# Kernel optimization log

Hardware: AMD Instinct MI355X
Metric: run time of the kernel (lower is better)

Reference implementation:

```python
import jax, jax.numpy as jnp
import numpy as np
from jax import lax

BN_EPS = 1e-5


def _conv(x, w):
    # stride-1, VALID conv; the torch 'locally connected' layer shares weights
    # across pixels, so it is exactly a standard conv2d.
    return lax.conv_general_dilated(
        x, w, window_strides=(1, 1), padding='VALID',
        dimension_numbers=('NCHW', 'OIHW', 'NCHW'))


def _batchnorm(x, gamma, beta):
    # training-mode BatchNorm2d: batch statistics over (N, H, W)
    mean = jnp.mean(x, axis=(0, 2, 3), keepdims=True)
    var = jnp.var(x, axis=(0, 2, 3), keepdims=True)
    xhat = (x - mean) * lax.rsqrt(var + BN_EPS)
    return xhat * gamma[None, :, None, None] + beta[None, :, None, None]


def setup_inputs() -> dict:
    key = jax.random.key(0)
    ks = jax.random.split(key, 6)
    B = 16384
    x = jax.random.normal(ks[0], (B, 256), dtype=jnp.float32)
    w1 = jax.random.normal(ks[1], (16, 1, 3, 3), dtype=jnp.float32)
    w2 = jax.random.normal(ks[2], (32, 16, 2, 2), dtype=jnp.float32)
    w3 = jax.random.normal(ks[3], (64, 32, 1, 1), dtype=jnp.float32)
    fan_in = 64 * 13 * 13
    bound = 1.0 / np.sqrt(fan_in)
    fc_w = jax.random.uniform(ks[4], (10, fan_in), minval=-bound, maxval=bound, dtype=jnp.float32)
    fc_b = jax.random.uniform(ks[5], (10,), minval=-bound, maxval=bound, dtype=jnp.float32)
    return {
        'x': x, 'w1': w1, 'w2': w2, 'w3': w3,
        'g1': jnp.ones((16,), jnp.float32), 'b1': jnp.zeros((16,), jnp.float32),
        'g2': jnp.ones((32,), jnp.float32), 'b2': jnp.zeros((32,), jnp.float32),
        'g3': jnp.ones((64,), jnp.float32), 'b3': jnp.zeros((64,), jnp.float32),
        'fc_w': fc_w, 'fc_b': fc_b,
    }


def reference(x, w1, w2, w3, g1, b1, g2, b2, g3, b3, fc_w, fc_b):
    h = x.reshape(-1, 1, 16, 16)                     # [B,1,16,16]
    h = jax.nn.relu(_batchnorm(_conv(h, w1), g1, b1))  # [B,16,14,14]
    h = jax.nn.relu(_batchnorm(_conv(h, w2), g2, b2))  # [B,32,13,13]
    h = jax.nn.relu(_batchnorm(_conv(h, w3), g3, b3))  # [B,64,13,13]
    h = h.reshape(h.shape[0], -1)                    # [B, 64*13*13]
    # dropout is identity in eval/deterministic mode
    return h @ fc_w.T + fc_b                         # [B,10]
```

## Files before the change

kernel.cpp:

```cpp
#include <hip/hip_runtime.h>


#define NPART 1024
#define P2_OFF 32768
#define ST_OFF 229376
#define ST1 ST_OFF
#define ST2 (ST_OFF + 32)
#define ST3 (ST_OFF + 96)
#define C2R_OFF 230400
#define C1R_OFF 231424
#define C2P_OFF 262144
#define A2G_BYTE 5242880ull
#define FCB_N 86528
#define A1S 24
#define A1B 384

typedef __attribute__((ext_vector_type(8))) short bf16x8;
typedef __attribute__((ext_vector_type(4))) float f32x4;
typedef __attribute__((ext_vector_type(4))) unsigned int u32x4;

__device__ __forceinline__ unsigned int f2bf(float f) {
  unsigned int u = __float_as_uint(f);
  return (u + 0x7fffu + ((u >> 16) & 1u)) >> 16;
}
__device__ __forceinline__ unsigned int pkbf(float a, float b) {
  unsigned ua = __float_as_uint(a) + 0x8000u;
  unsigned ub = __float_as_uint(b) + 0x8000u;
  return __builtin_amdgcn_perm(ub, ua, 0x07060302u);
}
__device__ __forceinline__ bf16x8 mkfrag(uint2 a, uint2 b) {
  u32x4 u = {a.x, a.y, b.x, b.y};
  return __builtin_bit_cast(bf16x8, u);
}

__device__ __forceinline__ void conv1_mfma(
    const float* __restrict__ sxi,
    short* dst,
    int r, int b, int q, bf16x8 a1f, f32x4 c1i)
{
  bf16x8 bf = {0, 0, 0, 0, 0, 0, 0, 0};
  unsigned* bu = (unsigned*)&bf;
  if (q == 0) {
    bu[0] = pkbf(sxi[r * 16 + b],           sxi[r * 16 + b + 1]);
    bu[1] = pkbf(sxi[r * 16 + b + 2],       sxi[(r + 1) * 16 + b]);
    bu[2] = pkbf(sxi[(r + 1) * 16 + b + 1], sxi[(r + 1) * 16 + b + 2]);
    bu[3] = pkbf(sxi[(r + 2) * 16 + b],     sxi[(r + 2) * 16 + b + 1]);
  } else if (q == 1) {
    bu[0] = pkbf(sxi[(r + 2) * 16 + b + 2], 0.f);
  }
  f32x4 acc = c1i;
  acc = __builtin_amdgcn_mfma_f32_16x16x32_bf16(a1f, bf, acc, 0, 0, 0);
  float v0 = acc[0] > 0.f ? acc[0] : 0.f;
  float v1 = acc[1] > 0.f ? acc[1] : 0.f;
  float v2 = acc[2] > 0.f ? acc[2] : 0.f;
  float v3 = acc[3] > 0.f ? acc[3] : 0.f;
  uint2 pk;
  pk.x = pkbf(v0, v1);
  pk.y = pkbf(v2, v3);
  *(uint2*)(dst + b * A1S + 4 * q) = pk;
}

__device__ __forceinline__ bf16x8 conv1_afrag(const float* w1, float rs1b,
                                              int b, int q) {
  bf16x8 v;
#pragma unroll
  for (int j = 0; j < 8; ++j) {
    int tap = 8 * q + j;
    v[j] = (tap < 9) ? (short)f2bf(w1[b * 9 + tap] * rs1b) : (short)0;
  }
  return v;
}

__global__ __launch_bounds__(256) void k1_xsyrk(
    const float* __restrict__ x, float* __restrict__ parts)
{
  __shared__ alignas(16) short sb[16 * 16 * 2 * 16];
  const int tid = threadIdx.x, w = tid >> 6, lane = tid & 63;
  const int b = lane & 15, q = lane >> 4;
  {
    const float4* xs = (const float4*)(x + (size_t)blockIdx.x * (16 * 256));
    for (int e = tid; e < 16 * 64; e += 256) {
      float4 v = xs[e];
      int img = e >> 6, row = (e >> 2) & 15, g = e & 3;
      uint2 pk;
      pk.x = pkbf(v.x, v.y);
      pk.y = pkbf(v.z, v.w);
      *(uint2*)(sb + ((img * 16 + row) * 2 + 0) * 16 + 4 * g) = pk;
    }
  }
  __syncthreads();
  {
    int img = tid >> 4, row = tid & 15;
    const unsigned* s0 = (const unsigned*)(sb + ((img * 16 + row) * 2 + 0) * 16);
    unsigned* s1 = (unsigned*)(sb + ((img * 16 + row) * 2 + 1) * 16);
    unsigned wprev = s0[0];
#pragma unroll
    for (int c = 0; c < 8; ++c) {
      unsigned wnext = (c < 7) ? s0[c + 1] : 0u;
      s1[c] = __builtin_amdgcn_perm(wnext, wprev, 0x05040302u);
      wprev = wnext;
    }
  }
  __syncthreads();
  const int di = (b < 9) ? (b / 3) : 0;
  const int dj = (b < 9) ? (b - di * 3) : 0;
  const int cp = dj & 1, dsh = dj >> 1;
  const int h = q >> 1, jb = (q & 1) * 8;
  const int wb = (jb >> 1) + dsh;
  f32x4 acc = {0.f, 0.f, 0.f, 0.f};
#pragma unroll 1
  for (int t = 0; t < 4; ++t) {
    const int ib = (w * 4 + t) * 16;
#pragma unroll 1
    for (int s = 0; s < 7; ++s) {
      bf16x8 af;
      unsigned* au = (unsigned*)&af;
      if (b < 9) {
        const unsigned* sr = (const unsigned*)(
            sb + ((ib + (2 * s + h + di)) * 2 + cp) * 16);
        au[0] = sr[wb];
        au[1] = sr[wb + 1];
        au[2] = sr[wb + 2];
        au[3] = (jb == 0) ? sr[wb + 3] : 0u;
      } else if (b == 9) {
#pragma unroll
        for (int cc = 0; cc < 4; ++cc) {
          unsigned lo = (jb + 2 * cc     < 14) ? 0x3F80u : 0u;
          unsigned hi = (jb + 2 * cc + 1 < 14) ? 0x3F800000u : 0u;
          au[cc] = lo | hi;
        }
      } else {
#pragma unroll
        for (int cc = 0; cc < 4; ++cc) au[cc] = 0u;
      }
      acc = __builtin_amdgcn_mfma_f32_16x16x32_bf16(af, af, acc, 0, 0, 0);
    }
  }
  __syncthreads();
  float* redc = (float*)sb;
#pragma unroll
  for (int rr = 0; rr < 4; ++rr)
    redc[w * 256 + (4 * q + rr) * 16 + b] = acc[rr];
  __syncthreads();
  parts[blockIdx.x * 256 + tid] =
      redc[tid] + redc[256 + tid] + redc[512 + tid] + redc[768 + tid];
}

__global__ __launch_bounds__(256) void k_stats1a(
    const float* __restrict__ parts, float* __restrict__ ws)
{
  const int e = blockIdx.x, tid = threadIdx.x;
  const int w = tid >> 6, lane = tid & 63;
  __shared__ float rs[4];
  float s = 0.f;
#pragma unroll 4
  for (int i = tid; i < 1024; i += 256) s += parts[i * 256 + e];
#pragma unroll
  for (int d = 1; d < 64; d <<= 1) s += __shfl_xor(s, d);
  if (lane == 0) rs[w] = s;
  __syncthreads();
  if (tid == 0) ws[C1R_OFF + e] = rs[0] + rs[1] + rs[2] + rs[3];
}

__global__ __launch_bounds__(64) void k_stats1b(
    const float* __restrict__ w1, const float* __restrict__ gamma,
    const float* __restrict__ beta, float* __restrict__ ws)
{
  const int c = threadIdx.x;
  if (c >= 16) return;
  const float* C = ws + C1R_OFF;
  float wr[9];
#pragma unroll
  for (int p = 0; p < 9; ++p) wr[p] = w1[c * 9 + p];
  float msum = 0.f;
#pragma unroll
  for (int p = 0; p < 9; ++p) msum += wr[p] * C[9 * 16 + p];
  float e2 = 0.f;
#pragma unroll
  for (int a = 0; a < 9; ++a)
#pragma unroll
    for (int bb = 0; bb < 9; ++bb)
      e2 += wr[a] * wr[bb] * C[a * 16 + bb];
  const float inv_n = 1.0f / (16384.0f * 196.0f);
  float mean = msum * inv_n;
  float var  = e2 * inv_n - mean * mean;
  float sv   = gamma[c] * rsqrtf(var + 1e-5f);
  ws[ST1 + c]      = sv;
  ws[ST1 + 16 + c] = beta[c] - mean * sv;
}

__global__ __launch_bounds__(256) void k_stats2(
    const float* __restrict__ gamma, const float* __restrict__ beta,
    float* __restrict__ ws, int nch, int part_off, int st_off, float inv_n)
{
  const int c = blockIdx.x, tid = threadIdx.x;
  const int w = tid >> 6, lane = tid & 63;
  __shared__ float rs[4], rq[4];
  float s = 0.f, q = 0.f;
#pragma unroll 4
  for (int i = tid; i < NPART; i += 256) {
    s += ws[part_off + i * 2 * nch + c];
    q += ws[part_off + i * 2 * nch + nch + c];
  }
#pragma unroll
  for (int d = 1; d < 64; d <<= 1) {
    s += __shfl_xor(s, d);
    q += __shfl_xor(q, d);
  }
  if (lane == 0) { rs[w] = s; rq[w] = q; }
  __syncthreads();
  if (tid == 0) {
    float st = rs[0] + rs[1] + rs[2] + rs[3];
    float qt = rq[0] + rq[1] + rq[2] + rq[3];
    float mean = st * inv_n;
    float var  = qt * inv_n - mean * mean;
    float sv   = gamma[c] * rsqrtf(var + 1e-5f);
    ws[st_off + c]       = sv;
    ws[st_off + nch + c] = beta[c] - mean * sv;
  }
}

__global__ __launch_bounds__(256) void k3_conv2_stats(
    const float* __restrict__ x, const float* __restrict__ w1,
    const float* __restrict__ w2, float* __restrict__ ws)
{
  __shared__ float sx_s[16 * 256 + 16];
  __shared__ alignas(16) short a1h[4 * 3 * A1B];
  __shared__ float redf[256];
  const int tid = threadIdx.x, w = tid >> 6, lane = tid & 63;
  const int b = lane & 15, q = lane >> 4;
  {
    const float4* xs = (const float4*)(x + (size_t)blockIdx.x * (16 * 256));
    float4* sd = (float4*)sx_s;
    for (int e = tid; e < 16 * 64; e += 256) sd[e] = xs[e];
    if (tid < 16) sx_s[16 * 256 + tid] = 0.f;
  }
  bf16x8 a1f = conv1_afrag(w1, ws[ST1 + b], b, q);
  f32x4 c1i;
#pragma unroll
  for (int r = 0; r < 4; ++r) c1i[r] = ws[ST1 + 16 + 4 * q + r];
  bf16x8 b2h[4];
#pragma unroll
  for (int ks = 0; ks < 2; ++ks)
#pragma unroll
    for (int nt = 0; nt < 2; ++nt) {
      bf16x8 vh;
#pragma unroll
      for (int j = 0; j < 8; ++j) {
        int kk = 8 * (q & 1) + j, dj = q >> 1;
        vh[j] = (short)f2bf(w2[(nt * 16 + b) * 64 + kk * 4 + ks * 2 + dj]);
      }
      b2h[ks * 2 + nt] = vh;
    }
  const float vb = (b < 13) ? 1.f : 0.f;
  const int colAr = (b + (q >> 1) < 15) ? (b + (q >> 1)) : 15;
  const int offAl = colAr * A1S + 8 * (q & 1);
  __syncthreads();

  float s2r[2][4] = {{0.f,0.f,0.f,0.f},{0.f,0.f,0.f,0.f}};
  float q2r[2][4] = {{0.f,0.f,0.f,0.f},{0.f,0.f,0.f,0.f}};
  short* pb0 = a1h + w * (3 * A1B);
  short* pb1 = pb0 + A1B;
  short* pb2 = pb0 + 2 * A1B;
#pragma unroll 1
  for (int t = 0; t < 4; ++t) {
    const float* sxi = sx_s + (w * 4 + t) * 256;
    conv1_mfma(sxi, pb0, 0, b, q, a1f, c1i);
    conv1_mfma(sxi, pb1, 1, b, q, a1f, c1i);
    __builtin_amdgcn_wave_barrier();
#pragma unroll 1
    for (int i = 0; i < 13; ++i) {
      if (i < 12) conv1_mfma(sxi, pb2, i + 2, b, q, a1f, c1i);
      bf16x8 ah0 = *(const bf16x8*)(pb0 + offAl);
      bf16x8 ah1 = *(const bf16x8*)(pb1 + offAl);
      f32x4 acc2[2] = {{0.f,0.f,0.f,0.f},{0.f,0.f,0.f,0.f}};
#pragma unroll
      for (int nt = 0; nt < 2; ++nt) {
        acc2[nt] = __builtin_amdgcn_mfma_f32_16x16x32_bf16(b2h[nt], ah0, acc2[nt], 0, 0, 0);
        acc2[nt] = __builtin_amdgcn_mfma_f32_16x16x32_bf16(b2h[2 + nt], ah1, acc2[nt], 0, 0, 0);
      }
#pragma unroll
      for (int nt = 0; nt < 2; ++nt)
#pragma unroll
        for (int r = 0; r < 4; ++r) {
          float ym = acc2[nt][r] * vb;
          s2r[nt][r] += ym;
          q2r[nt][r] = fmaf(ym, acc2[nt][r], q2r[nt][r]);
        }
      short* tpb = pb0; pb0 = pb1; pb1 = pb2; pb2 = tpb;
      __builtin_amdgcn_wave_barrier();
    }
  }
#pragma unroll
  for (int nt = 0; nt < 2; ++nt)
#pragma unroll
    for (int r = 0; r < 4; ++r) {
      float sv = s2r[nt][r], qv = q2r[nt][r];
      sv += __shfl_xor(sv, 1); sv += __shfl_xor(sv, 2);
      sv += __shfl_xor(sv, 4); sv += __shfl_xor(sv, 8);
      qv += __shfl_xor(qv, 1); qv += __shfl_xor(qv, 2);
      qv += __shfl_xor(qv, 4); qv += __shfl_xor(qv, 8);
      if (b == 0) {
        redf[w * 64 + nt * 16 + 4 * q + r]      = sv;
        redf[w * 64 + 32 + nt * 16 + 4 * q + r] = qv;
      }
    }
  __syncthreads();
  if (tid < 64)
    ws[P2_OFF + blockIdx.x * 64 + tid] =
        redf[tid] + redf[64 + tid] + redf[128 + tid] + redf[192 + tid];
}

__global__ __launch_bounds__(256) void k5_a2(
    const float* __restrict__ x, const float* __restrict__ w1,
    const float* __restrict__ w2, float* __restrict__ ws,
    short* __restrict__ a2g, float* __restrict__ parts)
{
  __shared__ float sx_s[16 * 256 + 16];
  __shared__ alignas(16) short a1h[4 * 3 * A1B];
  __shared__ alignas(16) short a2st[4 * 512];
  __shared__ float s2red[4 * 32];
  const int tid = threadIdx.x, w = tid >> 6, lane = tid & 63;
  const int b = lane & 15, q = lane >> 4;
  {
    const float4* xs = (const float4*)(x + (size_t)blockIdx.x * (16 * 256));
    float4* sd = (float4*)sx_s;
    for (int e = tid; e < 16 * 64; e += 256) sd[e] = xs[e];
    if (tid < 16) sx_s[16 * 256 + tid] = 0.f;
  }
  bf16x8 a1f = conv1_afrag(w1, ws[ST1 + b], b, q);
  f32x4 c1i;
#pragma unroll
  for (int r = 0; r < 4; ++r) c1i[r] = ws[ST1 + 16 + 4 * q + r];
  bf16x8 b2h[4];
#pragma unroll
  for (int ks = 0; ks < 2; ++ks)
#pragma unroll
    for (int nt = 0; nt < 2; ++nt) {
      float rs2b = ws[ST2 + nt * 16 + b];
      bf16x8 vh;
#pragma unroll
      for (int j = 0; j < 8; ++j) {
        int kk = 8 * (q & 1) + j, dj = q >> 1;
        vh[j] = (short)f2bf(w2[(nt * 16 + b) * 64 + kk * 4 + ks * 2 + dj] * rs2b);
      }
      b2h[ks * 2 + nt] = vh;
    }
  f32x4 c2i[2];
#pragma unroll
  for (int nt = 0; nt < 2; ++nt) {
    float t2b = ws[ST2 + 32 + nt * 16 + b];
#pragma unroll
    for (int r = 0; r < 4; ++r)
      c2i[nt][r] = (4 * q + r < 13) ? t2b : -1e30f;
  }
  const int colAr = (b + (q >> 1) < 15) ? (b + (q >> 1)) : 15;
  const int offAl = colAr * A1S + 8 * (q & 1);
  const u32x4 ou = {0x3F803F80u, 0x3F803F80u, 0x3F803F80u, 0x3F803F80u};
  const bf16x8 ones = __builtin_bit_cast(bf16x8, ou);
  __syncthreads();

  f32x4 accT0 = {0.f,0.f,0.f,0.f}, accT1 = {0.f,0.f,0.f,0.f},
        accT2 = {0.f,0.f,0.f,0.f};
  f32x4 accS0 = {0.f,0.f,0.f,0.f}, accS1 = {0.f,0.f,0.f,0.f};
  short* pb0 = a1h + w * (3 * A1B);
  short* pb1 = pb0 + A1B;
  short* pb2 = pb0 + 2 * A1B;
  short* st = a2st + w * 512;
#pragma unroll 1
  for (int t = 0; t < 4; ++t) {
    const int img = blockIdx.x * 16 + w * 4 + t;
    const float* sxi = sx_s + (w * 4 + t) * 256;
    short* gb = a2g + (size_t)img * 5408;
    conv1_mfma(sxi, pb0, 0, b, q, a1f, c1i);
    conv1_mfma(sxi, pb1, 1, b, q, a1f, c1i);
    __builtin_amdgcn_wave_barrier();
    uint2 pkp[2];
#pragma unroll 1
    for (int i = 0; i < 13; ++i) {
      if (i < 12) conv1_mfma(sxi, pb2, i + 2, b, q, a1f, c1i);
      bf16x8 ah0 = *(const bf16x8*)(pb0 + offAl);
      bf16x8 ah1 = *(const bf16x8*)(pb1 + offAl);
      uint2 pkc[2];
#pragma unroll
      for (int nt = 0; nt < 2; ++nt) {
        f32x4 acc2 = c2i[nt];
        acc2 = __builtin_amdgcn_mfma_f32_16x16x32_bf16(ah0, b2h[nt], acc2, 0, 0, 0);
        acc2 = __builtin_amdgcn_mfma_f32_16x16x32_bf16(ah1, b2h[2 + nt], acc2, 0, 0, 0);
        float v0 = acc2[0] > 0.f ? acc2[0] : 0.f;
        float v1 = acc2[1] > 0.f ? acc2[1] : 0.f;
        float v2 = acc2[2] > 0.f ? acc2[2] : 0.f;
        float v3 = acc2[3] > 0.f ? acc2[3] : 0.f;
        uint2 pk;
        pk.x = pkbf(v0, v1);
        pk.y = pkbf(v2, v3);
        short* sp = st + nt * 16 + b;
        sp[(4 * q + 0) * 32] = (short)pk.x;
        sp[(4 * q + 1) * 32] = (short)(pk.x >> 16);
        sp[(4 * q + 2) * 32] = (short)pk.y;
        sp[(4 * q + 3) * 32] = (short)(pk.y >> 16);
        pkc[nt] = pk;
      }
      __builtin_amdgcn_wave_barrier();
      if (lane < 52) {
        bf16x8 vv = *(const bf16x8*)(st + lane * 8);
        *(bf16x8*)(gb + (size_t)i * 416 + lane * 8) = vv;
      }
      if (i & 1) {
        bf16x8 xf0 = mkfrag(pkp[0], pkc[0]);
        bf16x8 xf1 = mkfrag(pkp[1], pkc[1]);
        accT0 = __builtin_amdgcn_mfma_f32_16x16x32_bf16(xf0, xf0, accT0, 0, 0, 0);
        accT1 = __builtin_amdgcn_mfma_f32_16x16x32_bf16(xf0, xf1, accT1, 0, 0, 0);
        accT2 = __builtin_amdgcn_mfma_f32_16x16x32_bf16(xf1, xf1, accT2, 0, 0, 0);
        accS0 = __builtin_amdgcn_mfma_f32_16x16x32_bf16(ones, xf0, accS0, 0, 0, 0);
        accS1 = __builtin_amdgcn_mfma_f32_16x16x32_bf16(ones, xf1, accS1, 0, 0, 0);
      } else {
        pkp[0] = pkc[0];
        pkp[1] = pkc[1];
      }
      short* tpb = pb0; pb0 = pb1; pb1 = pb2; pb2 = tpb;
      __builtin_amdgcn_wave_barrier();
    }
    {
      uint2 zz; zz.x = 0u; zz.y = 0u;
      bf16x8 xf0 = mkfrag(pkp[0], zz);
      bf16x8 xf1 = mkfrag(pkp[1], zz);
      accT0 = __builtin_amdgcn_mfma_f32_16x16x32_bf16(xf0, xf0, accT0, 0, 0, 0);
      accT1 = __builtin_amdgcn_mfma_f32_16x16x32_bf16(xf0, xf1, accT1, 0, 0, 0);
      accT2 = __builtin_amdgcn_mfma_f32_16x16x32_bf16(xf1, xf1, accT2, 0, 0, 0);
      accS0 = __builtin_amdgcn_mfma_f32_16x16x32_bf16(ones, xf0, accS0, 0, 0, 0);
      accS1 = __builtin_amdgcn_mfma_f32_16x16x32_bf16(ones, xf1, accS1, 0, 0, 0);
    }
  }
  if (q == 0) {
    s2red[w * 32 + b]      = accS0[0];
    s2red[w * 32 + 16 + b] = accS1[0];
  }
  float* redc = sx_s;
#pragma unroll
  for (int rr = 0; rr < 4; ++rr) {
    int m = 4 * q + rr;
    redc[w * 1024 + 0   + m * 16 + b] = accT0[rr];
    redc[w * 1024 + 256 + m * 16 + b] = accT1[rr];
    redc[w * 1024 + 512 + m * 16 + b] = accT2[rr];
  }
  __syncthreads();
  for (int e = tid; e < 768; e += 256)
    parts[blockIdx.x * 800 + e] =
        redc[e] + redc[1024 + e] + redc[2048 + e] + redc[3072 + e];
  if (tid < 32)
    parts[blockIdx.x * 800 + 768 + tid] =
        s2red[tid] + s2red[32 + tid] + s2red[64 + tid] + s2red[96 + tid];
}

__global__ __launch_bounds__(256) void k_statsC(
    const float* __restrict__ parts, float* __restrict__ ws)
{
  const int e = blockIdx.x, tid = threadIdx.x;
  const int w = tid >> 6, lane = tid & 63;
  __shared__ float rs[4];
  float s = 0.f;
#pragma unroll 4
  for (int i = tid; i < 1024; i += 256) s += parts[i * 800 + e];
#pragma unroll
  for (int d = 1; d < 64; d <<= 1) s += __shfl_xor(s, d);
  if (lane == 0) rs[w] = s;
  __syncthreads();
  if (tid == 0) ws[C2R_OFF + e] = rs[0] + rs[1] + rs[2] + rs[3];
}

__global__ __launch_bounds__(64) void k_stats3n(
    const float* __restrict__ w3, const float* __restrict__ gamma,
    const float* __restrict__ beta, float* __restrict__ ws)
{
  const int c3 = threadIdx.x;
  if (c3 >= 64) return;
  const float* C2R = ws + C2R_OFF;
  float wr[32];
#pragma unroll
  for (int k = 0; k < 32; ++k) wr[k] = w3[c3 * 32 + k];
  const float inv_n = 1.0f / (16384.0f * 169.0f);
  float msum = 0.f;
#pragma unroll
  for (int k = 0; k < 32; ++k) msum += wr[k] * C2R[768 + k];
  float e2 = 0.f;
  for (int a = 0; a < 16; ++a)
#pragma unroll
    for (int bb = 0; bb < 16; ++bb) {
      e2 += wr[a] * wr[bb] * C2R[a * 16 + bb];
      e2 += wr[16 + a] * wr[16 + bb] * C2R[512 + a * 16 + bb];
      e2 += 2.f * wr[a] * wr[16 + bb] * C2R[256 + a * 16 + bb];
    }
  float mean = msum * inv_n;
  float var  = e2 * inv_n - mean * mean;
  float sv   = gamma[c3] * rsqrtf(var + 1e-5f);
  ws[ST3 + c3]      = sv;
  ws[ST3 + 64 + c3] = beta[c3] - mean * sv;
}

__global__ __launch_bounds__(256) void k0_fcB(
    const float* __restrict__ fcw, unsigned int* __restrict__ fcB)
{
  int f = blockIdx.x * 256 + threadIdx.x;
  int u = f & 3, lane = (f >> 2) & 63, h = (f >> 8) & 1, p = f >> 9;
  int b = lane & 15, q = lane >> 4;
  unsigned lo = 0, hi = 0;
  if (b < 10) {
    int c30 = h * 32 + (u >> 1) * 16 + 4 * q + 2 * (u & 1);
    lo = f2bf(fcw[b * 10816 + c30 * 169 + p]);
    hi = f2bf(fcw[b * 10816 + (c30 + 1) * 169 + p]);
  }
  fcB[f] = lo | (hi << 16);
}

__global__ __launch_bounds__(256) void k7_fc(
    const short* __restrict__ a2g, const float* __restrict__ w3,
    const float* __restrict__ fcb, const float* __restrict__ ws,
    float* __restrict__ out)
{
  __shared__ float redf7[1024];
  const int tid = threadIdx.x, w = tid >> 6, lane = tid & 63;
  const int b = lane & 15, q = lane >> 4;
  bf16x8 b3h[4];
  f32x4 c3i[4];
#pragma unroll
  for (int nt = 0; nt < 4; ++nt) {
    float s3 = ws[ST3 + nt * 16 + b];
    bf16x8 vh;
#pragma unroll
    for (int j = 0; j < 8; ++j)
      vh[j] = (short)f2bf(w3[(nt * 16 + b) * 32 + 8 * q + j] * s3);
    b3h[nt] = vh;
#pragma unroll
    for (int r = 0; r < 4; ++r)
      c3i[nt][r] = ws[ST3 + 64 + nt * 16 + 4 * q + r];
  }
  const bf16x8* fcB = (const bf16x8*)ws;
  const short* abase = a2g + (size_t)(blockIdx.x * 16 + b) * 5408 + 8 * q;
  const int p0 = (w * 169) >> 2, p1 = ((w + 1) * 169) >> 2;
  f32x4 aF0 = {0.f, 0.f, 0.f, 0.f}, aF1 = {0.f, 0.f, 0.f, 0.f};
  bf16x8 vpre = *(const bf16x8*)(abase + p0 * 32);
  bf16x8 bw0 = fcB[(p0 * 2 + 0) * 64 + lane];
  bf16x8 bw1 = fcB[(p0 * 2 + 1) * 64 + lane];
#pragma unroll 1
  for (int p = p0; p < p1; ++p) {
    bf16x8 vc = vpre, f0 = bw0, f1 = bw1;
    if (p + 1 < p1) {
      vpre = *(const bf16x8*)(abase + (p + 1) * 32);
      bw0 = fcB[((p + 1) * 2 + 0) * 64 + lane];
      bw1 = fcB[((p + 1) * 2 + 1) * 64 + lane];
    }
    uint2 pkc[4];
#pragma unroll
    for (int nt = 0; nt < 4; ++nt) {
      f32x4 acc3 = c3i[nt];
      acc3 = __builtin_amdgcn_mfma_f32_16x16x32_bf16(b3h[nt], vc, acc3, 0, 0, 0);
      float v0 = acc3[0] > 0.f ? acc3[0] : 0.f;
      float v1 = acc3[1] > 0.f ? acc3[1] : 0.f;
      float v2 = acc3[2] > 0.f ? acc3[2] : 0.f;
      float v3 = acc3[3] > 0.f ? acc3[3] : 0.f;
      pkc[nt].x = pkbf(v0, v1);
      pkc[nt].y = pkbf(v2, v3);
    }
    aF0 = __builtin_amdgcn_mfma_f32_16x16x32_bf16(mkfrag(pkc[0], pkc[1]), f0, aF0, 0, 0, 0);
    aF1 = __builtin_amdgcn_mfma_f32_16x16x32_bf16(mkfrag(pkc[2], pkc[3]), f1, aF1, 0, 0, 0);
  }
#pragma unroll
  for (int r = 0; r < 4; ++r)
    redf7[w * 256 + (4 * q + r) * 16 + b] = aF0[r] + aF1[r];
  __syncthreads();
  if (tid < 160) {
    int img = tid / 10, jj = tid - img * 10;
    float s = redf7[img * 16 + jj] + redf7[256 + img * 16 + jj] +
              redf7[512 + img * 16 + jj] + redf7[768 + img * 16 + jj];
    out[(blockIdx.x * 16 + img) * 10 + jj] = s + fcb[jj];
  }
}

extern "C" void kernel_launch(void* const* d_in, const int* in_sizes, int n_in,
                              void* d_out, int out_size, void* d_ws, size_t ws_size,
                              hipStream_t stream) {
  (void)in_sizes; (void)n_in; (void)out_size; (void)ws_size;
  const float* x   = (const float*)d_in[0];
  const float* w1  = (const float*)d_in[1];
  const float* w2  = (const float*)d_in[2];
  const float* w3  = (const float*)d_in[3];
  const float* g1  = (const float*)d_in[4];
  const float* b1  = (const float*)d_in[5];
  const float* g2  = (const float*)d_in[6];
  const float* b2  = (const float*)d_in[7];
  const float* g3  = (const float*)d_in[8];
  const float* b3  = (const float*)d_in[9];
  const float* fcw = (const float*)d_in[10];
  const float* fcb = (const float*)d_in[11];
  float* out = (float*)d_out;
  float* ws  = (float*)d_ws;
  short* a2g = (short*)((char*)d_ws + A2G_BYTE);
  float* parts = ws + C2P_OFF;

  k1_xsyrk<<<1024, 256, 0, stream>>>(x, parts);
  k_stats1a<<<256, 256, 0, stream>>>(parts, ws);
  k_stats1b<<<1, 64, 0, stream>>>(w1, g1, b1, ws);
  k3_conv2_stats<<<1024, 256, 0, stream>>>(x, w1, w2, ws);
  k_stats2<<<32, 256, 0, stream>>>(g2, b2, ws, 32, P2_OFF, ST2,
                                   1.0f / (16384.0f * 169.0f));
  k5_a2<<<1024, 256, 0, stream>>>(x, w1, w2, ws, a2g, parts);
  k_statsC<<<800, 256, 0, stream>>>(parts, ws);
  k_stats3n<<<1, 64, 0, stream>>>(w3, g3, b3, ws);
  k0_fcB<<<FCB_N / 256, 256, 0, stream>>>(fcw, (unsigned int*)ws);
  k7_fc<<<1024, 256, 0, stream>>>(a2g, w3, fcb, ws, out);
}
```

Measured before the change: 256.4 us.

## Materialize conv1 activations in k3 and reuse them in k5 instead of recomputing

The conv2-stats kernel now also writes the bf16 conv1 activations (BN1+ReLU applied) to a workspace buffer. A new k5 variant reads those activations instead of recomputing conv1 from x. This trades recomputing conv1 MFMA work for extra global writes and reads, about 117MB of bf16 traffic. The new path is chosen only when the workspace is large enough, otherwise the old kernels run.

Result: no change. 256.5 us (+0.0%).

```diff
diff --git a/kernel.cpp b/kernel.cpp
--- a/kernel.cpp
+++ b/kernel.cpp
@@ -271,6 +271,111 @@
 #pragma unroll 1
     for (int i = 0; i < 13; ++i) {
       if (i < 12) conv1_mfma(sxi, pb2, i + 2, b, q, a1f, c1i);
+      bf16x8 ah0 = *(const bf16x8*)(pb0 + offAl);
+      bf16x8 ah1 = *(const bf16x8*)(pb1 + offAl);
+      f32x4 acc2[2] = {{0.f,0.f,0.f,0.f},{0.f,0.f,0.f,0.f}};
+#pragma unroll
+      for (int nt = 0; nt < 2; ++nt) {
+        acc2[nt] = __builtin_amdgcn_mfma_f32_16x16x32_bf16(b2h[nt], ah0, acc2[nt], 0, 0, 0);
+        acc2[nt] = __builtin_amdgcn_mfma_f32_16x16x32_bf16(b2h[2 + nt], ah1, acc2[nt], 0, 0, 0);
+      }
+#pragma unroll
+      for (int nt = 0; nt < 2; ++nt)
+#pragma unroll
+        for (int r = 0; r < 4; ++r) {
+          float ym = acc2[nt][r] * vb;
+          s2r[nt][r] += ym;
+          q2r[nt][r] = fmaf(ym, acc2[nt][r], q2r[nt][r]);
+        }
+      short* tpb = pb0; pb0 = pb1; pb1 = pb2; pb2 = tpb;
+      __builtin_amdgcn_wave_barrier();
+    }
+  }
+#pragma unroll
+  for (int nt = 0; nt < 2; ++nt)
+#pragma unroll
+    for (int r = 0; r < 4; ++r) {
+      float sv = s2r[nt][r], qv = q2r[nt][r];
+      sv += __shfl_xor(sv, 1); sv += __shfl_xor(sv, 2);
+      sv += __shfl_xor(sv, 4); sv += __shfl_xor(sv, 8);
+      qv += __shfl_xor(qv, 1); qv += __shfl_xor(qv, 2);
+      qv += __shfl_xor(qv, 4); qv += __shfl_xor(qv, 8);
+      if (b == 0) {
+        redf[w * 64 + nt * 16 + 4 * q + r]      = sv;
+        redf[w * 64 + 32 + nt * 16 + 4 * q + r] = qv;
+      }
+    }
+  __syncthreads();
+  if (tid < 64)
+    ws[P2_OFF + blockIdx.x * 64 + tid] =
+        redf[tid] + redf[64 + tid] + redf[128 + tid] + redf[192 + tid];
+}
+
+__global__ __launch_bounds__(256) void k3_v2(
+    const float* __restrict__ x, const float* __restrict__ w1,
+    const float* __restrict__ w2, float* __restrict__ ws,
+    short* __restrict__ a1g)
+{
+  __shared__ float sx_s[16 * 256 + 16];
+  __shared__ alignas(16) short a1h[4 * 3 * A1B];
+  __shared__ float redf[256];
+  const int tid = threadIdx.x, w = tid >> 6, lane = tid & 63;
+  const int b = lane & 15, q = lane >> 4;
+  {
+    const float4* xs = (const float4*)(x + (size_t)blockIdx.x * (16 * 256));
+    float4* sd = (float4*)sx_s;
+    for (int e = tid; e < 16 * 64; e += 256) sd[e] = xs[e];
+    if (tid < 16) sx_s[16 * 256 + tid] = 0.f;
+  }
+  bf16x8 a1f = conv1_afrag(w1, ws[ST1 + b], b, q);
+  f32x4 c1i;
+#pragma unroll
+  for (int r = 0; r < 4; ++r) c1i[r] = ws[ST1 + 16 + 4 * q + r];
+  bf16x8 b2h[4];
+#pragma unroll
+  for (int ks = 0; ks < 2; ++ks)
+#pragma unroll
+    for (int nt = 0; nt < 2; ++nt) {
+      bf16x8 vh;
+#pragma unroll
+      for (int j = 0; j < 8; ++j) {
+        int kk = 8 * (q & 1) + j, dj = q >> 1;
+        vh[j] = (short)f2bf(w2[(nt * 16 + b) * 64 + kk * 4 + ks * 2 + dj]);
+      }
+      b2h[ks * 2 + nt] = vh;
+    }
+  const float vb = (b < 13) ? 1.f : 0.f;
+  const int colAr = (b + (q >> 1) < 15) ? (b + (q >> 1)) : 15;
+  const int offAl = colAr * A1S + 8 * (q & 1);
+  const int sco = (lane >> 1) * A1S + (lane & 1) * 8;
+  __syncthreads();
+
+  float s2r[2][4] = {{0.f,0.f,0.f,0.f},{0.f,0.f,0.f,0.f}};
+  float q2r[2][4] = {{0.f,0.f,0.f,0.f},{0.f,0.f,0.f,0.f}};
+  short* pb0 = a1h + w * (3 * A1B);
+  short* pb1 = pb0 + A1B;
+  short* pb2 = pb0 + 2 * A1B;
+#pragma unroll 1
+  for (int t = 0; t < 4; ++t) {
+    const int img = blockIdx.x * 16 + w * 4 + t;
+    short* ag = a1g + (size_t)img * 3584;
+    const float* sxi = sx_s + (w * 4 + t) * 256;
+    conv1_mfma(sxi, pb0, 0, b, q, a1f, c1i);
+    conv1_mfma(sxi, pb1, 1, b, q, a1f, c1i);
+    __builtin_amdgcn_wave_barrier();
+    if (lane < 32) {
+      *(bf16x8*)(ag + 0 * 256 + lane * 8) = *(const bf16x8*)(pb0 + sco);
+      *(bf16x8*)(ag + 1 * 256 + lane * 8) = *(const bf16x8*)(pb1 + sco);
+    }
+#pragma unroll 1
+    for (int i = 0; i < 13; ++i) {
+      if (i < 12) {
+        conv1_mfma(sxi, pb2, i + 2, b, q, a1f, c1i);
+        __builtin_amdgcn_wave_barrier();
+        if (lane < 32)
+          *(bf16x8*)(ag + (size_t)(i + 2) * 256 + lane * 8) =
+              *(const bf16x8*)(pb2 + sco);
+      }
       bf16x8 ah0 = *(const bf16x8*)(pb0 + offAl);
       bf16x8 ah1 = *(const bf16x8*)(pb1 + offAl);
       f32x4 acc2[2] = {{0.f,0.f,0.f,0.f},{0.f,0.f,0.f,0.f}};
@@ -453,6 +558,132 @@
         s2red[tid] + s2red[32 + tid] + s2red[64 + tid] + s2red[96 + tid];
 }
 
+__global__ __launch_bounds__(256) void k5_v2(
+    const short* __restrict__ a1g, const float* __restrict__ w2,
+    float* __restrict__ ws, short* __restrict__ a2g,
+    float* __restrict__ parts)
+{
+  __shared__ float redc_s[4096];
+  __shared__ alignas(16) short a2st[4 * 512];
+  __shared__ float s2red[4 * 32];
+  const int tid = threadIdx.x, w = tid >> 6, lane = tid & 63;
+  const int b = lane & 15, q = lane >> 4;
+  bf16x8 b2h[4];
+#pragma unroll
+  for (int ks = 0; ks < 2; ++ks)
+#pragma unroll
+    for (int nt = 0; nt < 2; ++nt) {
+      float rs2b = ws[ST2 + nt * 16 + b];
+      bf16x8 vh;
+#pragma unroll
+      for (int j = 0; j < 8; ++j) {
+        int kk = 8 * (q & 1) + j, dj = q >> 1;
+        vh[j] = (short)f2bf(w2[(nt * 16 + b) * 64 + kk * 4 + ks * 2 + dj] * rs2b);
+      }
+      b2h[ks * 2 + nt] = vh;
+    }
+  f32x4 c2i[2];
+#pragma unroll
+  for (int nt = 0; nt < 2; ++nt) {
+    float t2b = ws[ST2 + 32 + nt * 16 + b];
+#pragma unroll
+    for (int r = 0; r < 4; ++r)
+      c2i[nt][r] = (4 * q + r < 13) ? t2b : -1e30f;
+  }
+  const int colAr = (b + (q >> 1) < 15) ? (b + (q >> 1)) : 15;
+  const int loff = colAr * 16 + (q & 1) * 8;
+  const u32x4 ou = {0x3F803F80u, 0x3F803F80u, 0x3F803F80u, 0x3F803F80u};
+  const bf16x8 ones = __builtin_bit_cast(bf16x8, ou);
+
+  f32x4 accT0 = {0.f,0.f,0.f,0.f}, accT1 = {0.f,0.f,0.f,0.f},
+        accT2 = {0.f,0.f,0.f,0.f};
+  f32x4 accS0 = {0.f,0.f,0.f,0.f}, accS1 = {0.f,0.f,0.f,0.f};
+  short* st = a2st + w * 512;
+#pragma unroll 1
+  for (int t = 0; t < 4; ++t) {
+    const int img = blockIdx.x * 16 + w * 4 + t;
+    const short* ag = a1g + (size_t)img * 3584 + loff;
+    short* gb = a2g + (size_t)img * 5408;
+    bf16x8 rA = *(const bf16x8*)(ag);
+    bf16x8 rB = *(const bf16x8*)(ag + 256);
+    bf16x8 rC = *(const bf16x8*)(ag + 512);
+    uint2 pkp[2];
+#pragma unroll 1
+    for (int i = 0; i < 13; ++i) {
+      bf16x8 ah0 = rA, ah1 = rB;
+      rA = rB; rB = rC;
+      if (i <= 10) rC = *(const bf16x8*)(ag + (size_t)(i + 3) * 256);
+      uint2 pkc[2];
+#pragma unroll
+      for (int nt = 0; nt < 2; ++nt) {
+        f32x4 acc2 = c2i[nt];
+        acc2 = __builtin_amdgcn_mfma_f32_16x16x32_bf16(ah0, b2h[nt], acc2, 0, 0, 0);
+        acc2 = __builtin_amdgcn_mfma_f32_16x16x32_bf16(ah1, b2h[2 + nt], acc2, 0, 0, 0);
+        float v0 = acc2[0] > 0.f ? acc2[0] : 0.f;
+        float v1 = acc2[1] > 0.f ? acc2[1] : 0.f;
+        float v2 = acc2[2] > 0.f ? acc2[2] : 0.f;
+        float v3 = acc2[3] > 0.f ? acc2[3] : 0.f;
+        uint2 pk;
+        pk.x = pkbf(v0, v1);
+        pk.y = pkbf(v2, v3);
+        short* sp = st + nt * 16 + b;
+        sp[(4 * q + 0) * 32] = (short)pk.x;
+        sp[(4 * q + 1) * 32] = (short)(pk.x >> 16);
+        sp[(4 * q + 2) * 32] = (short)pk.y;
+        sp[(4 * q + 3) * 32] = (short)(pk.y >> 16);
+        pkc[nt] = pk;
+      }
+      __builtin_amdgcn_wave_barrier();
+      if (lane < 52) {
+        bf16x8 vv = *(const bf16x8*)(st + lane * 8);
+        *(bf16x8*)(gb + (size_t)i * 416 + lane * 8) = vv;
+      }
+      if (i & 1) {
+        bf16x8 xf0 = mkfrag(pkp[0], pkc[0]);
+        bf16x8 xf1 = mkfrag(pkp[1], pkc[1]);
+        accT0 = __builtin_amdgcn_mfma_f32_16x16x32_bf16(xf0, xf0, accT0, 0, 0, 0);
+        accT1 = __builtin_amdgcn_mfma_f32_16x16x32_bf16(xf0, xf1, accT1, 0, 0, 0);
+        accT2 = __builtin_amdgcn_mfma_f32_16x16x32_bf16(xf1, xf1, accT2, 0, 0, 0);
+        accS0 = __builtin_amdgcn_mfma_f32_16x16x32_bf16(ones, xf0, accS0, 0, 0, 0);
+        accS1 = __builtin_amdgcn_mfma_f32_16x16x32_bf16(ones, xf1, accS1, 0, 0, 0);
+      } else {
+        pkp[0] = pkc[0];
+        pkp[1] = pkc[1];
+      }
+      __builtin_amdgcn_wave_barrier();
+    }
+    {
+      uint2 zz; zz.x = 0u; zz.y = 0u;
+      bf16x8 xf0 = mkfrag(pkp[0], zz);
+      bf16x8 xf1 = mkfrag(pkp[1], zz);
+      accT0 = __builtin_amdgcn_mfma_f32_16x16x32_bf16(xf0, xf0, accT0, 0, 0, 0);
+      accT1 = __builtin_amdgcn_mfma_f32_16x16x32_bf16(xf0, xf1, accT1, 0, 0, 0);
+      accT2 = __builtin_amdgcn_mfma_f32_16x16x32_bf16(xf1, xf1, accT2, 0, 0, 0);
+      accS0 = __builtin_amdgcn_mfma_f32_16x16x32_bf16(ones, xf0, accS0, 0, 0, 0);
+      accS1 = __builtin_amdgcn_mfma_f32_16x16x32_bf16(ones, xf1, accS1, 0, 0, 0);
+    }
+  }
+  if (q == 0) {
+    s2red[w * 32 + b]      = accS0[0];
+    s2red[w * 32 + 16 + b] = accS1[0];
+  }
+  float* redc = redc_s;
+#pragma unroll
+  for (int rr = 0; rr < 4; ++rr) {
+    int m = 4 * q + rr;
+    redc[w * 1024 + 0   + m * 16 + b] = accT0[rr];
+    redc[w * 1024 + 256 + m * 16 + b] = accT1[rr];
+    redc[w * 1024 + 512 + m * 16 + b] = accT2[rr];
+  }
+  __syncthreads();
+  for (int e = tid; e < 768; e += 256)
+    parts[blockIdx.x * 800 + e] =
+        redc[e] + redc[1024 + e] + redc[2048 + e] + redc[3072 + e];
+  if (tid < 32)
+    parts[blockIdx.x * 800 + 768 + tid] =
+        s2red[tid] + s2red[32 + tid] + s2red[64 + tid] + s2red[96 + tid];
+}
+
 __global__ __launch_bounds__(256) void k_statsC(
     const float* __restrict__ parts, float* __restrict__ ws)
 {
@@ -580,7 +811,7 @@
 extern "C" void kernel_launch(void* const* d_in, const int* in_sizes, int n_in,
                               void* d_out, int out_size, void* d_ws, size_t ws_size,
                               hipStream_t stream) {
-  (void)in_sizes; (void)n_in; (void)out_size; (void)ws_size;
+  (void)in_sizes; (void)n_in; (void)out_size;
   const float* x   = (const float*)d_in[0];
   const float* w1  = (const float*)d_in[1];
   const float* w2  = (const float*)d_in[2];
@@ -597,14 +828,19 @@
   float* ws  = (float*)d_ws;
   short* a2g = (short*)((char*)d_ws + A2G_BYTE);
   float* parts = ws + C2P_OFF;
+  const size_t a1off = A2G_BYTE + 16384ull * 5408ull * 2ull;
+  short* a1g = (short*)((char*)d_ws + a1off);
+  const int big = ws_size >= a1off + 16384ull * 7168ull;
 
   k1_xsyrk<<<1024, 256, 0, stream>>>(x, parts);
   k_stats1a<<<256, 256, 0, stream>>>(parts, ws);
   k_stats1b<<<1, 64, 0, stream>>>(w1, g1, b1, ws);
-  k3_conv2_stats<<<1024, 256, 0, stream>>>(x, w1, w2, ws);
+  if (big) k3_v2<<<1024, 256, 0, stream>>>(x, w1, w2, ws, a1g);
+  else     k3_conv2_stats<<<1024, 256, 0, stream>>>(x, w1, w2, ws);
   k_stats2<<<32, 256, 0, stream>>>(g2, b2, ws, 32, P2_OFF, ST2,
                                    1.0f / (16384.0f * 169.0f));
-  k5_a2<<<1024, 256, 0, stream>>>(x, w1, w2, ws, a2g, parts);
+  if (big) k5_v2<<<1024, 256, 0, stream>>>(a1g, w2, ws, a2g, parts);
+  else     k5_a2<<<1024, 256, 0, stream>>>(x, w1, w2, ws, a2g, parts);
   k_statsC<<<800, 256, 0, stream>>>(parts, ws);
   k_stats3n<<<1, 64, 0, stream>>>(w3, g3, b3, ws);
   k0_fcB<<<FCB_N / 256, 256, 0, stream>>>(fcw, (unsigned int*)ws);
```

## Cache conv1 activations in workspace to skip recomputing conv1 in the a2 kernel

Applied to the files above, without the earlier changes.

The conv2-stats kernel now writes the bf16 conv1 output (post BN/ReLU) for each image to a global workspace buffer, as far as the workspace size allows. The a2 kernel then reads these cached activations instead of reloading x and recomputing conv1 with MFMA, and falls back to recomputation for uncached images. This trades recompute for extra global writes and reads of about 7 KB per image, and the payoff depends on ws_size being large enough. The float-to-bf16 pack also switches to the hardware v_cvt_pk_bf16_f32 instruction, which rounds differently from the old add-and-truncate.

Result: slower. 295.9 us (+15.4%).

```diff
diff --git a/kernel.cpp b/kernel.cpp
--- a/kernel.cpp
+++ b/kernel.cpp
@@ -24,9 +24,9 @@
   return (u + 0x7fffu + ((u >> 16) & 1u)) >> 16;
 }
 __device__ __forceinline__ unsigned int pkbf(float a, float b) {
-  unsigned ua = __float_as_uint(a) + 0x8000u;
-  unsigned ub = __float_as_uint(b) + 0x8000u;
-  return __builtin_amdgcn_perm(ub, ua, 0x07060302u);
+  unsigned int r;
+  asm("v_cvt_pk_bf16_f32 %0, %1, %2" : "=v"(r) : "v"(a), "v"(b));
+  return r;
 }
 __device__ __forceinline__ bf16x8 mkfrag(uint2 a, uint2 b) {
   u32x4 u = {a.x, a.y, b.x, b.y};
@@ -69,6 +69,62 @@
     v[j] = (tap < 9) ? (short)f2bf(w1[b * 9 + tap] * rs1b) : (short)0;
   }
   return v;
+}
+
+struct SyrkAcc { f32x4 T0, T1, T2, S0, S1; };
+__device__ __forceinline__ void conv2_step(
+    bf16x8 ah0, bf16x8 ah1, const bf16x8* b2h, const f32x4* c2i,
+    short* st, short* gb, int i, int b, int q, int lane,
+    uint2* pkp, SyrkAcc& A, bf16x8 ones)
+{
+  uint2 pkc[2];
+#pragma unroll
+  for (int nt = 0; nt < 2; ++nt) {
+    f32x4 acc2 = c2i[nt];
+    acc2 = __builtin_amdgcn_mfma_f32_16x16x32_bf16(ah0, b2h[nt], acc2, 0, 0, 0);
+    acc2 = __builtin_amdgcn_mfma_f32_16x16x32_bf16(ah1, b2h[2 + nt], acc2, 0, 0, 0);
+    float v0 = acc2[0] > 0.f ? acc2[0] : 0.f;
+    float v1 = acc2[1] > 0.f ? acc2[1] : 0.f;
+    float v2 = acc2[2] > 0.f ? acc2[2] : 0.f;
+    float v3 = acc2[3] > 0.f ? acc2[3] : 0.f;
+    uint2 pk;
+    pk.x = pkbf(v0, v1);
+    pk.y = pkbf(v2, v3);
+    short* sp = st + nt * 16 + b;
+    sp[(4 * q + 0) * 32] = (short)pk.x;
+    sp[(4 * q + 1) * 32] = (short)(pk.x >> 16);
+    sp[(4 * q + 2) * 32] = (short)pk.y;
+    sp[(4 * q + 3) * 32] = (short)(pk.y >> 16);
+    pkc[nt] = pk;
+  }
+  __builtin_amdgcn_wave_barrier();
+  if (lane < 52) {
+    bf16x8 vv = *(const bf16x8*)(st + lane * 8);
+    *(bf16x8*)(gb + (size_t)i * 416 + lane * 8) = vv;
+  }
+  if (i & 1) {
+    bf16x8 xf0 = mkfrag(pkp[0], pkc[0]);
+    bf16x8 xf1 = mkfrag(pkp[1], pkc[1]);
+    A.T0 = __builtin_amdgcn_mfma_f32_16x16x32_bf16(xf0, xf0, A.T0, 0, 0, 0);
+    A.T1 = __builtin_amdgcn_mfma_f32_16x16x32_bf16(xf0, xf1, A.T1, 0, 0, 0);
+    A.T2 = __builtin_amdgcn_mfma_f32_16x16x32_bf16(xf1, xf1, A.T2, 0, 0, 0);
+    A.S0 = __builtin_amdgcn_mfma_f32_16x16x32_bf16(ones, xf0, A.S0, 0, 0, 0);
+    A.S1 = __builtin_amdgcn_mfma_f32_16x16x32_bf16(ones, xf1, A.S1, 0, 0, 0);
+  } else {
+    pkp[0] = pkc[0];
+    pkp[1] = pkc[1];
+  }
+  __builtin_amdgcn_wave_barrier();
+}
+__device__ __forceinline__ void syrk_tail(uint2* pkp, SyrkAcc& A, bf16x8 ones) {
+  uint2 zz; zz.x = 0u; zz.y = 0u;
+  bf16x8 xf0 = mkfrag(pkp[0], zz);
+  bf16x8 xf1 = mkfrag(pkp[1], zz);
+  A.T0 = __builtin_amdgcn_mfma_f32_16x16x32_bf16(xf0, xf0, A.T0, 0, 0, 0);
+  A.T1 = __builtin_amdgcn_mfma_f32_16x16x32_bf16(xf0, xf1, A.T1, 0, 0, 0);
+  A.T2 = __builtin_amdgcn_mfma_f32_16x16x32_bf16(xf1, xf1, A.T2, 0, 0, 0);
+  A.S0 = __builtin_amdgcn_mfma_f32_16x16x32_bf16(ones, xf0, A.S0, 0, 0, 0);
+  A.S1 = __builtin_amdgcn_mfma_f32_16x16x32_bf16(ones, xf1, A.S1, 0, 0, 0);
 }
 
 __global__ __launch_bounds__(256) void k1_xsyrk(
@@ -220,15 +276,17 @@
   }
 }
 
-__global__ __launch_bounds__(256) void k3_conv2_stats(
+__global__ __launch_bounds__(256) void k3_v2(
     const float* __restrict__ x, const float* __restrict__ w1,
-    const float* __restrict__ w2, float* __restrict__ ws)
+    const float* __restrict__ w2, float* __restrict__ ws,
+    short* __restrict__ a1g, int cached)
 {
   __shared__ float sx_s[16 * 256 + 16];
   __shared__ alignas(16) short a1h[4 * 3 * A1B];
   __shared__ float redf[256];
   const int tid = threadIdx.x, w = tid >> 6, lane = tid & 63;
   const int b = lane & 15, q = lane >> 4;
+  const bool doStore = (int)blockIdx.x < (cached >> 4);
   {
     const float4* xs = (const float4*)(x + (size_t)blockIdx.x * (16 * 256));
     float4* sd = (float4*)sx_s;
@@ -255,6 +313,7 @@
   const float vb = (b < 13) ? 1.f : 0.f;
   const int colAr = (b + (q >> 1) < 15) ? (b + (q >> 1)) : 15;
   const int offAl = colAr * A1S + 8 * (q & 1);
+  const int sco = (lane >> 1) * A1S + (lane & 1) * 8;
   __syncthreads();
 
   float s2r[2][4] = {{0.f,0.f,0.f,0.f},{0.f,0.f,0.f,0.f}};
@@ -264,13 +323,25 @@
   short* pb2 = pb0 + 2 * A1B;
 #pragma unroll 1
   for (int t = 0; t < 4; ++t) {
+    const int img = blockIdx.x * 16 + w * 4 + t;
+    short* ag = a1g + (size_t)img * 3584;
     const float* sxi = sx_s + (w * 4 + t) * 256;
     conv1_mfma(sxi, pb0, 0, b, q, a1f, c1i);
     conv1_mfma(sxi, pb1, 1, b, q, a1f, c1i);
     __builtin_amdgcn_wave_barrier();
+    if (doStore && lane < 32) {
+      *(bf16x8*)(ag + 0 * 256 + lane * 8) = *(const bf16x8*)(pb0 + sco);
+      *(bf16x8*)(ag + 1 * 256 + lane * 8) = *(const bf16x8*)(pb1 + sco);
+    }
 #pragma unroll 1
     for (int i = 0; i < 13; ++i) {
-      if (i < 12) conv1_mfma(sxi, pb2, i + 2, b, q, a1f, c1i);
+      if (i < 12) {
+        conv1_mfma(sxi, pb2, i + 2, b, q, a1f, c1i);
+        __builtin_amdgcn_wave_barrier();
+        if (doStore && lane < 32)
+          *(bf16x8*)(ag + (size_t)(i + 2) * 256 + lane * 8) =
+              *(const bf16x8*)(pb2 + sco);
+      }
       bf16x8 ah0 = *(const bf16x8*)(pb0 + offAl);
       bf16x8 ah1 = *(const bf16x8*)(pb1 + offAl);
       f32x4 acc2[2] = {{0.f,0.f,0.f,0.f},{0.f,0.f,0.f,0.f}};
@@ -311,10 +382,11 @@
         redf[tid] + redf[64 + tid] + redf[128 + tid] + redf[192 + tid];
 }
 
-__global__ __launch_bounds__(256) void k5_a2(
+__global__ __launch_bounds__(256) void k5_v2(
     const float* __restrict__ x, const float* __restrict__ w1,
-    const float* __restrict__ w2, float* __restrict__ ws,
-    short* __restrict__ a2g, float* __restrict__ parts)
+    const short* __restrict__ a1g, const float* __restrict__ w2,
+    float* __restrict__ ws, short* __restrict__ a2g,
+    float* __restrict__ parts, int cached)
 {
   __shared__ float sx_s[16 * 256 + 16];
   __shared__ alignas(16) short a1h[4 * 3 * A1B];
@@ -322,16 +394,20 @@
   __shared__ float s2red[4 * 32];
   const int tid = threadIdx.x, w = tid >> 6, lane = tid & 63;
   const int b = lane & 15, q = lane >> 4;
-  {
+  const bool useCache = (int)blockIdx.x < (cached >> 4);
+  if (!useCache) {
     const float4* xs = (const float4*)(x + (size_t)blockIdx.x * (16 * 256));
     float4* sd = (float4*)sx_s;
     for (int e = tid; e < 16 * 64; e += 256) sd[e] = xs[e];
     if (tid < 16) sx_s[16 * 256 + tid] = 0.f;
   }
-  bf16x8 a1f = conv1_afrag(w1, ws[ST1 + b], b, q);
-  f32x4 c1i;
-#pragma unroll
-  for (int r = 0; r < 4; ++r) c1i[r] = ws[ST1 + 16 + 4 * q + r];
+  bf16x8 a1f = {0,0,0,0,0,0,0,0};
+  f32x4 c1i = {0.f, 0.f, 0.f, 0.f};
+  if (!useCache) {
+    a1f = conv1_afrag(w1, ws[ST1 + b], b, q);
+#pragma unroll
+    for (int r = 0; r < 4; ++r) c1i[r] = ws[ST1 + 16 + 4 * q + r];
+  }
   bf16x8 b2h[4];
 #pragma unroll
   for (int ks = 0; ks < 2; ++ks)
@@ -356,93 +432,68 @@
   }
   const int colAr = (b + (q >> 1) < 15) ? (b + (q >> 1)) : 15;
   const int offAl = colAr * A1S + 8 * (q & 1);
+  const int loff  = colAr * 16  + (q & 1) * 8;
   const u32x4 ou = {0x3F803F80u, 0x3F803F80u, 0x3F803F80u, 0x3F803F80u};
   const bf16x8 ones = __builtin_bit_cast(bf16x8, ou);
   __syncthreads();
 
-  f32x4 accT0 = {0.f,0.f,0.f,0.f}, accT1 = {0.f,0.f,0.f,0.f},
-        accT2 = {0.f,0.f,0.f,0.f};
-  f32x4 accS0 = {0.f,0.f,0.f,0.f}, accS1 = {0.f,0.f,0.f,0.f};
-  short* pb0 = a1h + w * (3 * A1B);
-  short* pb1 = pb0 + A1B;
-  short* pb2 = pb0 + 2 * A1B;
+  SyrkAcc A;
+  A.T0 = A.T1 = A.T2 = A.S0 = A.S1 = (f32x4){0.f, 0.f, 0.f, 0.f};
   short* st = a2st + w * 512;
-#pragma unroll 1
-  for (int t = 0; t < 4; ++t) {
-    const int img = blockIdx.x * 16 + w * 4 + t;
-    const float* sxi = sx_s + (w * 4 + t) * 256;
-    short* gb = a2g + (size_t)img * 5408;
-    conv1_mfma(sxi, pb0, 0, b, q, a1f, c1i);
-    conv1_mfma(sxi, pb1, 1, b, q, a1f, c1i);
-    __builtin_amdgcn_wave_barrier();
-    uint2 pkp[2];
-#pragma unroll 1
-    for (int i = 0; i < 13; ++i) {
-      if (i < 12) conv1_mfma(sxi, pb2, i + 2, b, q, a1f, c1i);
-      bf16x8 ah0 = *(const bf16x8*)(pb0 + offAl);
-      bf16x8 ah1 = *(const bf16x8*)(pb1 + offAl);
-      uint2 pkc[2];
-#pragma unroll
-      for (int nt = 0; nt < 2; ++nt) {
-        f32x4 acc2 = c2i[nt];
-        acc2 = __builtin_amdgcn_mfma_f32_16x16x32_bf16(ah0, b2h[nt], acc2, 0, 0, 0);
-        acc2 = __builtin_amdgcn_mfma_f32_16x16x32_bf16(ah1, b2h[2 + nt], acc2, 0, 0, 0);
-        float v0 = acc2[0] > 0.f ? acc2[0] : 0.f;
-        float v1 = acc2[1] > 0.f ? acc2[1] : 0.f;
-        float v2 = acc2[2] > 0.f ? acc2[2] : 0.f;
-        float v3 = acc2[3] > 0.f ? acc2[3] : 0.f;
-        uint2 pk;
-        pk.x = pkbf(v0, v1);
-        pk.y = pkbf(v2, v3);
-        short* sp = st + nt * 16 + b;
-        sp[(4 * q + 0) * 32] = (short)pk.x;
-        sp[(4 * q + 1) * 32] = (short)(pk.x >> 16);
-        sp[(4 * q + 2) * 32] = (short)pk.y;
-        sp[(4 * q + 3) * 32] = (short)(pk.y >> 16);
-        pkc[nt] = pk;
-      }
+  if (useCache) {
+#pragma unroll 1
+    for (int t = 0; t < 4; ++t) {
+      const int img = blockIdx.x * 16 + w * 4 + t;
+      const short* ag = a1g + (size_t)img * 3584 + loff;
+      short* gb = a2g + (size_t)img * 5408;
+      bf16x8 rA = *(const bf16x8*)(ag);
+      bf16x8 rB = *(const bf16x8*)(ag + 256);
+      bf16x8 rC = *(const bf16x8*)(ag + 512);
+      uint2 pkp[2];
+#pragma unroll 1
+      for (int i = 0; i < 13; ++i) {
+        bf16x8 ah0 = rA, ah1 = rB;
+        rA = rB; rB = rC;
+        if (i <= 10) rC = *(const bf16x8*)(ag + (size_t)(i + 3) * 256);
+        conv2_step(ah0, ah1, b2h, c2i, st, gb, i, b, q, lane, pkp, A, ones);
+      }
+      syrk_tail(pkp, A, ones);
+    }
+  } else {
+    short* pb0 = a1h + w * (3 * A1B);
+    short* pb1 = pb0 + A1B;
+    short* pb2 = pb0 + 2 * A1B;
+#pragma unroll 1
+    for (int t = 0; t < 4; ++t) {
+      const int img = blockIdx.x * 16 + w * 4 + t;
+      const float* sxi = sx_s + (w * 4 + t) * 256;
+      short* gb = a2g + (size_t)img * 5408;
+      conv1_mfma(sxi, pb0, 0, b, q, a1f, c1i);
+      conv1_mfma(sxi, pb1, 1, b, q, a1f, c1i);
       __builtin_amdgcn_wave_barrier();
-      if (lane < 52) {
-        bf16x8 vv = *(const bf16x8*)(st + lane * 8);
-        *(bf16x8*)(gb + (size_t)i * 416 + lane * 8) = vv;
-      }
-      if (i & 1) {
-        bf16x8 xf0 = mkfrag(pkp[0], pkc[0]);
-        bf16x8 xf1 = mkfrag(pkp[1], pkc[1]);
-        accT0 = __builtin_amdgcn_mfma_f32_16x16x32_bf16(xf0, xf0, accT0, 0, 0, 0);
-        accT1 = __builtin_amdgcn_mfma_f32_16x16x32_bf16(xf0, xf1, accT1, 0, 0, 0);
-        accT2 = __builtin_amdgcn_mfma_f32_16x16x32_bf16(xf1, xf1, accT2, 0, 0, 0);
-        accS0 = __builtin_amdgcn_mfma_f32_16x16x32_bf16(ones, xf0, accS0, 0, 0, 0);
-        accS1 = __builtin_amdgcn_mfma_f32_16x16x32_bf16(ones, xf1, accS1, 0, 0, 0);
-      } else {
-        pkp[0] = pkc[0];
-        pkp[1] = pkc[1];
-      }
-      short* tpb = pb0; pb0 = pb1; pb1 = pb2; pb2 = tpb;
-      __builtin_amdgcn_wave_barrier();
-    }
-    {
-      uint2 zz; zz.x = 0u; zz.y = 0u;
-      bf16x8 xf0 = mkfrag(pkp[0], zz);
-      bf16x8 xf1 = mkfrag(pkp[1], zz);
-      accT0 = __builtin_amdgcn_mfma_f32_16x16x32_bf16(xf0, xf0, accT0, 0, 0, 0);
-      accT1 = __builtin_amdgcn_mfma_f32_16x16x32_bf16(xf0, xf1, accT1, 0, 0, 0);
-      accT2 = __builtin_amdgcn_mfma_f32_16x16x32_bf16(xf1, xf1, accT2, 0, 0, 0);
-      accS0 = __builtin_amdgcn_mfma_f32_16x16x32_bf16(ones, xf0, accS0, 0, 0, 0);
-      accS1 = __builtin_amdgcn_mfma_f32_16x16x32_bf16(ones, xf1, accS1, 0, 0, 0);
+      uint2 pkp[2];
+#pragma unroll 1
+      for (int i = 0; i < 13; ++i) {
+        if (i < 12) conv1_mfma(sxi, pb2, i + 2, b, q, a1f, c1i);
+        bf16x8 ah0 = *(const bf16x8*)(pb0 + offAl);
+        bf16x8 ah1 = *(const bf16x8*)(pb1 + offAl);
+        conv2_step(ah0, ah1, b2h, c2i, st, gb, i, b, q, lane, pkp, A, ones);
+        short* tpb = pb0; pb0 = pb1; pb1 = pb2; pb2 = tpb;
+      }
+      syrk_tail(pkp, A, ones);
     }
   }
   if (q == 0) {
-    s2red[w * 32 + b]      = accS0[0];
-    s2red[w * 32 + 16 + b] = accS1[0];
+    s2red[w * 32 + b]      = A.S0[0];
+    s2red[w * 32 + 16 + b] = A.S1[0];
   }
   float* redc = sx_s;
 #pragma unroll
   for (int rr = 0; rr < 4; ++rr) {
     int m = 4 * q + rr;
-    redc[w * 1024 + 0   + m * 16 + b] = accT0[rr];
-    redc[w * 1024 + 256 + m * 16 + b] = accT1[rr];
-    redc[w * 1024 + 512 + m * 16 + b] = accT2[rr];
+    redc[w * 1024 + 0   + m * 16 + b] = A.T0[rr];
+    redc[w * 1024 + 256 + m * 16 + b] = A.T1[rr];
+    redc[w * 1024 + 512 + m * 16 + b] = A.T2[rr];
   }
   __syncthreads();
   for (int e = tid; e < 768; e += 256)
@@ -580,7 +631,7 @@
 extern "C" void kernel_launch(void* const* d_in, const int* in_sizes, int n_in,
                               void* d_out, int out_size, void* d_ws, size_t ws_size,
                               hipStream_t stream) {
-  (void)in_sizes; (void)n_in; (void)out_size; (void)ws_size;
+  (void)in_sizes; (void)n_in; (void)out_size;
   const float* x   = (const float*)d_in[0];
   const float* w1  = (const float*)d_in[1];
   const float* w2  = (const float*)d_in[2];
@@ -597,14 +648,22 @@
   float* ws  = (float*)d_ws;
   short* a2g = (short*)((char*)d_ws + A2G_BYTE);
   float* parts = ws + C2P_OFF;
+  const size_t a1off = A2G_BYTE + 16384ull * 5408ull * 2ull;
+  short* a1g = (short*)((char*)d_ws + a1off);
+  int cached = 0;
+  if (ws_size > a1off) {
+    long long c = (long long)(ws_size - a1off) / 7168;
+    if (c > 16384) c = 16384;
+    cached = (int)c & ~15;
+  }
 
   k1_xsyrk<<<1024, 256, 0, stream>>>(x, parts);
   k_stats1a<<<256, 256, 0, stream>>>(parts, ws);
   k_stats1b<<<1, 64, 0, stream>>>(w1, g1, b1, ws);
-  k3_conv2_stats<<<1024, 256, 0, stream>>>(x, w1, w2, ws);
+  k3_v2<<<1024, 256, 0, stream>>>(x, w1, w2, ws, a1g, cached);
   k_stats2<<<32, 256, 0, stream>>>(g2, b2, ws, 32, P2_OFF, ST2,
                                    1.0f / (16384.0f * 169.0f));
-  k5_a2<<<1024, 256, 0, stream>>>(x, w1, w2, ws, a2g, parts);
+  k5_v2<<<1024, 256, 0, stream>>>(x, w1, a1g, w2, ws, a2g, parts, cached);
   k_statsC<<<800, 256, 0, stream>>>(parts, ws);
   k_stats3n<<<1, 64, 0, stream>>>(w3, g3, b3, ws);
   k0_fcB<<<FCB_N / 256, 256, 0, stream>>>(fcw, (unsigned int*)ws);
```
